# Performance work log

Hardware: AMD Instinct MI355X
Metric: run time of the kernel (lower is better)

## Reference

```python
import jax, jax.numpy as jnp
import numpy as np

NEG_SLOPE_GAT = 0.2   # PyG GATConv default negative_slope
NEG_SLOPE = 0.01      # torch.nn.LeakyReLU default
NUM_AISLES = 20       # aisle_nrs drawn from [0,20); matches aisle_nrs.max()+1


def leaky(x, s):
    return jnp.where(x >= 0, x, s * x)


def gat_conv(x, src, dst, W, a_src, a_dst, b, n_nodes):
    """Single-head PyG GATConv (self-loops already appended to src/dst)."""
    h = x @ W                                        # [N, C]
    es = h @ a_src                                   # [N]
    ed = h @ a_dst                                   # [N]
    e = leaky(es[src] + ed[dst], NEG_SLOPE_GAT)      # [E] per-edge score
    m = jax.ops.segment_max(e, dst, num_segments=n_nodes)
    w = jnp.exp(e - m[dst])
    z = jax.ops.segment_sum(w, dst, num_segments=n_nodes)
    alpha = w / z[dst]                               # segment softmax over incoming edges
    out = jax.ops.segment_sum(h[src] * alpha[:, None], dst, num_segments=n_nodes)
    return out + b


def setup_inputs() -> dict:
    key = jax.random.key(0)
    ks = jax.random.split(key, 32)
    B, N, E = 16, 2048, 32768
    Fin, H, O, HA = 32, 128, 64, 256

    def glorot(k, shape):
        fan = shape[0] + shape[-1]
        return jax.random.uniform(k, shape, jnp.float32, -1.0, 1.0) * np.sqrt(6.0 / fan)

    inp = {
        "graph_nodes": jax.random.normal(ks[0], (B, N, Fin), jnp.float32),
        "aisle_nrs": jax.random.randint(ks[1], (B, N), 0, NUM_AISLES),
        "graph_edge_links": jax.random.randint(ks[2], (B, 2, E), 0, N),
        "mask": jax.random.randint(ks[3], (B, N), 0, 2),
        "picks_left": jax.random.randint(ks[4], (B,), 0, 100),
        # GAT layer 1: Fin -> H
        "W1": glorot(ks[5], (Fin, H)), "as1": glorot(ks[6], (H,)), "ad1": glorot(ks[7], (H,)), "b1": jnp.zeros((H,), jnp.float32),
        # GAT layer 2: H -> H
        "W2": glorot(ks[8], (H, H)), "as2": glorot(ks[9], (H,)), "ad2": glorot(ks[10], (H,)), "b2": jnp.zeros((H,), jnp.float32),
        # GAT layer 3: H -> O
        "W3": glorot(ks[11], (H, O)), "as3": glorot(ks[12], (O,)), "ad3": glorot(ks[13], (O,)), "b3": jnp.zeros((O,), jnp.float32),
        # post-embedding MLP head
        "lw1": glorot(ks[14], (2 * O, HA)), "lb1": jnp.zeros((HA,), jnp.float32),
        "lw2": glorot(ks[15], (HA, O)), "lb2": jnp.zeros((O,), jnp.float32),
        "lw3": glorot(ks[16], (O, 1)), "lb3": jnp.zeros((1,), jnp.float32),
    }
    return inp


def reference(graph_nodes, aisle_nrs, graph_edge_links, mask, picks_left,
              W1, as1, ad1, b1, W2, as2, ad2, b2, W3, as3, ad3, b3,
              lw1, lb1, lw2, lb2, lw3, lb3):
    B, N, Fin = graph_nodes.shape
    NT = B * N
    x = graph_nodes.reshape(NT, Fin)

    # batch the graphs: offset per-graph edge indices, append self-loops
    off = (jnp.arange(B) * N)[:, None]
    src = (graph_edge_links[:, 0, :] + off).reshape(-1)
    dst = (graph_edge_links[:, 1, :] + off).reshape(-1)
    loops = jnp.arange(NT)
    src = jnp.concatenate([src, loops])
    dst = jnp.concatenate([dst, loops])

    x = gat_conv(x, src, dst, W1, as1, ad1, b1, NT)
    x = gat_conv(x, src, dst, W2, as2, ad2, b2, NT)
    x = gat_conv(x, src, dst, W3, as3, ad3, b3, NT)

    # scatter-mean aisle embedding
    batch_idx = jnp.repeat(jnp.arange(B), N)
    aid = aisle_nrs.reshape(-1) + batch_idx * NUM_AISLES   # [NT]
    S = B * NUM_AISLES
    ssum = jax.ops.segment_sum(x, aid, num_segments=S)
    cnt = jax.ops.segment_sum(jnp.ones((NT,), x.dtype), aid, num_segments=S)
    emb = ssum / jnp.maximum(cnt, 1.0)[:, None]

    x = jnp.concatenate([x, emb[aid]], axis=1)             # [NT, 2*O]
    x = leaky(x @ lw1 + lb1, NEG_SLOPE)
    x = leaky(x @ lw2 + lb2, NEG_SLOPE)
    x = (x @ lw3 + lb3).reshape(B, N)

    logits = jnp.where(mask != 0, x, -jnp.inf)
    return jax.nn.softmax(logits, axis=1)
```

## Files before the change

kernel.cpp:

```cpp
#include <hip/hip_runtime.h>
#include <hip/hip_bf16.h>
#include <math.h>

#define BATCH 16
#define NNODE 2048
#define EPG   32768
#define NT    (BATCH * NNODE)
#define ET    (BATCH * EPG + NT)
#define NUM_AISLES 20
#define SEG   (BATCH * NUM_AISLES)
#define NEG_GAT 0.2f
#define NEG_MLP 0.01f
#define ACHUNK 8
#define CAP 64

typedef __attribute__((ext_vector_type(8))) short s16x8;
typedef __attribute__((ext_vector_type(4))) float f32x4;

__device__ __forceinline__ void split_bf16(float v, unsigned short& hi, unsigned short& lo) {
    unsigned int u = __float_as_uint(v);
    unsigned int r = u + 0x7FFFu + ((u >> 16) & 1u);
    hi = (unsigned short)(r >> 16);
    float fh = __uint_as_float(((unsigned int)hi) << 16);
    float rem = v - fh;
    unsigned int u2 = __float_as_uint(rem);
    unsigned int r2 = u2 + 0x7FFFu + ((u2 >> 16) & 1u);
    lo = (unsigned short)(r2 >> 16);
}

__device__ __forceinline__ void decode_edge(int e, const int* __restrict__ links,
                                            int& s, int& d) {
    if (e < BATCH * EPG) {
        int b = e >> 15;
        int i = e & (EPG - 1);
        const int* pb = links + (size_t)b * 2 * EPG;
        s = pb[i] + (b << 11);
        d = pb[EPG + i] + (b << 11);
    } else {
        s = d = e - BATCH * EPG;
    }
}

__global__ __launch_bounds__(256) void edge_scatter(const int* __restrict__ links,
                                                    int* __restrict__ cnt,
                                                    int* __restrict__ col_bkt) {
    int e = blockIdx.x * 256 + threadIdx.x;
    if (e >= ET) return;
    int s, d;
    decode_edge(e, links, s, d);
    int pos = atomicAdd(&cnt[d], 1);
    if (pos < CAP) col_bkt[d * CAP + pos] = s;
}

template <int K, int NOUT, int COLS, bool LEAKY, bool ATTN, bool FINAL, bool CONCAT>
__global__ __launch_bounds__(256) void gemm_mfma(const float* __restrict__ A,
                                                 const float* __restrict__ W,
                                                 const float* __restrict__ bias,
                                                 float* __restrict__ out,
                                                 const float* __restrict__ a_src,
                                                 const float* __restrict__ a_dst,
                                                 float* __restrict__ es,
                                                 float* __restrict__ ed,
                                                 const float* __restrict__ emb,
                                                 const int* __restrict__ aisle,
                                                 const float* __restrict__ lw3,
                                                 const float* __restrict__ lb3,
                                                 const int* __restrict__ mask,
                                                 float* __restrict__ logits) {
    constexpr int BM = 64;
    constexpr int C = COLS / 16;
    constexpr int LDA = 40;

    __shared__ unsigned short Ah[BM * LDA], Al[BM * LDA];
    __shared__ unsigned short Wh[COLS * LDA], Wl[COLS * LDA];

    const int tid = threadIdx.x;
    const int wave = tid >> 6, lane = tid & 63;
    const int quad = lane >> 4, l15 = lane & 15;
    const int row0 = blockIdx.x * BM;
    const int c0 = blockIdx.y * COLS;

    f32x4 acc[C];
#pragma unroll
    for (int c = 0; c < C; ++c)
#pragma unroll
        for (int v = 0; v < 4; ++v) acc[c][v] = 0.f;

    const int arow = tid >> 2;
    const int aq = tid & 3;

    for (int kc = 0; kc < K; kc += 32) {
        {
            const int node = row0 + arow;
            const int off = kc + aq * 8;
            const float* srcp;
            if constexpr (CONCAT) {
                if (off < 64) {
                    srcp = A + (size_t)node * 64 + off;
                } else {
                    int g = node >> 11;
                    srcp = emb + ((size_t)(g * NUM_AISLES + aisle[node])) * 64 + (off - 64);
                }
            } else {
                srcp = A + (size_t)node * K + off;
            }
            unsigned short* dh = Ah + arow * LDA + aq * 8;
            unsigned short* dl = Al + arow * LDA + aq * 8;
#pragma unroll
            for (int q = 0; q < 2; ++q) {
                float4 v = ((const float4*)srcp)[q];
                unsigned short h0, l0, h1, l1, h2, l2, h3, l3;
                split_bf16(v.x, h0, l0);
                split_bf16(v.y, h1, l1);
                split_bf16(v.z, h2, l2);
                split_bf16(v.w, h3, l3);
                dh[q * 4 + 0] = h0; dh[q * 4 + 1] = h1; dh[q * 4 + 2] = h2; dh[q * 4 + 3] = h3;
                dl[q * 4 + 0] = l0; dl[q * 4 + 1] = l1; dl[q * 4 + 2] = l2; dl[q * 4 + 3] = l3;
            }
        }
        for (int i = tid; i < 32 * COLS; i += 256) {
            int k = i / COLS;
            int n = i - k * COLS;
            unsigned short h, l;
            split_bf16(W[(size_t)(kc + k) * NOUT + c0 + n], h, l);
            Wh[n * LDA + k] = h;
            Wl[n * LDA + k] = l;
        }
        __syncthreads();
        {
            int m = wave * 16 + l15;
            s16x8 ah = *(const s16x8*)&Ah[m * LDA + quad * 8];
            s16x8 al = *(const s16x8*)&Al[m * LDA + quad * 8];
#pragma unroll
            for (int c = 0; c < C; ++c) {
                int n = c * 16 + l15;
                s16x8 wh = *(const s16x8*)&Wh[n * LDA + quad * 8];
                s16x8 wl = *(const s16x8*)&Wl[n * LDA + quad * 8];
                acc[c] = __builtin_amdgcn_mfma_f32_16x16x32_bf16(ah, wh, acc[c], 0, 0, 0);
                acc[c] = __builtin_amdgcn_mfma_f32_16x16x32_bf16(ah, wl, acc[c], 0, 0, 0);
                acc[c] = __builtin_amdgcn_mfma_f32_16x16x32_bf16(al, wh, acc[c], 0, 0, 0);
            }
        }
        __syncthreads();
    }
    if constexpr (FINAL) {
#pragma unroll
        for (int reg = 0; reg < 4; ++reg) {
            float p = 0.f;
#pragma unroll
            for (int c = 0; c < C; ++c) {
                int colx = c * 16 + l15;
                float v = acc[c][reg] + bias[colx];
                v = v >= 0.f ? v : NEG_MLP * v;
                p += v * lw3[colx];
            }
#pragma unroll
            for (int mk = 1; mk < 16; mk <<= 1) p += __shfl_xor(p, mk, 64);
            if (l15 == 0) {
                int row = row0 + wave * 16 + quad * 4 + reg;
                float lg = p + lb3[0];
                logits[row] = (mask[row] != 0) ? lg : -INFINITY;
            }
        }
    } else {
#pragma unroll
        for (int c = 0; c < C; ++c) {
            int colx = c0 + c * 16 + l15;
            float bv = bias ? bias[colx] : 0.f;
#pragma unroll
            for (int reg = 0; reg < 4; ++reg) {
                int row = row0 + wave * 16 + quad * 4 + reg;
                float v = acc[c][reg] + bv;
                if (LEAKY) v = v >= 0.f ? v : NEG_MLP * v;
                out[(size_t)row * NOUT + colx] = v;
            }
        }
        if constexpr (ATTN) {
#pragma unroll
            for (int reg = 0; reg < 4; ++reg) {
                float ps = 0.f, pd = 0.f;
#pragma unroll
                for (int c = 0; c < C; ++c) {
                    int colx = c * 16 + l15;
                    float v = acc[c][reg];
                    ps += v * a_src[colx];
                    pd += v * a_dst[colx];
                }
#pragma unroll
                for (int mk = 1; mk < 16; mk <<= 1) {
                    ps += __shfl_xor(ps, mk, 64);
                    pd += __shfl_xor(pd, mk, 64);
                }
                if (l15 == 0) {
                    int row = row0 + wave * 16 + quad * 4 + reg;
                    es[row] = ps;
                    ed[row] = pd;
                }
            }
        }
    }
}

template <int HD>
__global__ __launch_bounds__(256) void gat_aggregate(const float* __restrict__ h,
                                                     const float* __restrict__ es,
                                                     const float* __restrict__ ed,
                                                     const int* __restrict__ cnt,
                                                     const int* __restrict__ col_bkt,
                                                     const float* __restrict__ bias,
                                                     float* __restrict__ out) {
    int node = (blockIdx.x * 256 + threadIdx.x) >> 6;
    int lane = threadIdx.x & 63;
    if (node >= NT) return;
    int deg = cnt[node];
    deg = deg < CAP ? deg : CAP;
    float edv = ed[node];

    float e0 = -INFINITY;
    int c0v = 0;
    if (lane < deg) {
        c0v = col_bkt[node * CAP + lane];
        float e = es[c0v] + edv;
        e0 = e >= 0.f ? e : NEG_GAT * e;
    }
    float m = e0;
#pragma unroll
    for (int off = 32; off; off >>= 1) m = fmaxf(m, __shfl_xor(m, off, 64));
    float z = __expf(e0 - m);
#pragma unroll
    for (int off = 32; off; off >>= 1) z += __shfl_xor(z, off, 64);
    float w0 = __expf(e0 - m) / z;

    int half = lane >> 5;
    int l31 = lane & 31;
    if (HD == 128) {
        float ax = 0.f, ay = 0.f, az = 0.f, aw = 0.f;
        for (int jj = 0; jj < deg; jj += 2) {
            int j2 = jj + half;
            int s = __shfl(c0v, j2, 64);
            float w = __shfl(w0, j2, 64);
            float4 v = *(const float4*)(h + (size_t)s * 128 + l31 * 4);
            ax += w * v.x; ay += w * v.y; az += w * v.z; aw += w * v.w;
        }
        ax += __shfl_xor(ax, 32, 64);
        ay += __shfl_xor(ay, 32, 64);
        az += __shfl_xor(az, 32, 64);
        aw += __shfl_xor(aw, 32, 64);
        if (half == 0) {
            float4 bv = *(const float4*)(bias + l31 * 4);
            float4 o;
            o.x = ax + bv.x; o.y = ay + bv.y; o.z = az + bv.z; o.w = aw + bv.w;
            *(float4*)(out + (size_t)node * 128 + l31 * 4) = o;
        }
    } else {
        float ax = 0.f, ay = 0.f;
        for (int jj = 0; jj < deg; jj += 2) {
            int j2 = jj + half;
            int s = __shfl(c0v, j2, 64);
            float w = __shfl(w0, j2, 64);
            float2 v = *(const float2*)(h + (size_t)s * 64 + l31 * 2);
            ax += w * v.x; ay += w * v.y;
        }
        ax += __shfl_xor(ax, 32, 64);
        ay += __shfl_xor(ay, 32, 64);
        if (half == 0) {
            float2 bv = *(const float2*)(bias + l31 * 2);
            float2 o;
            o.x = ax + bv.x; o.y = ay + bv.y;
            *(float2*)(out + (size_t)node * 64 + l31 * 2) = o;
        }
    }
}

__global__ __launch_bounds__(256) void aisle_partial(const float* __restrict__ x3,
                                                     const int* __restrict__ aisle,
                                                     float* __restrict__ psum,
                                                     int* __restrict__ pcnt) {
    int g = blockIdx.x >> 3;
    int ch = blockIdx.x & 7;
    int f = threadIdx.x & 63;
    int stripe = threadIdx.x >> 6;

    __shared__ float sacc[4][NUM_AISLES][64];
    __shared__ int scnt[4][NUM_AISLES];
    for (int i = threadIdx.x; i < 4 * NUM_AISLES * 64; i += 256)
        ((float*)sacc)[i] = 0.f;
    for (int i = threadIdx.x; i < 4 * NUM_AISLES; i += 256)
        ((int*)scnt)[i] = 0;
    __syncthreads();

    const int* ai = aisle + g * NNODE;
    const float* xg = x3 + (size_t)g * NNODE * 64;
    int n0 = ch * 256 + stripe * 64;
#pragma unroll 4
    for (int i = 0; i < 64; ++i) {
        int n = n0 + i;
        int a = ai[n];
        float v = xg[(size_t)n * 64 + f];
        sacc[stripe][a][f] += v;
        if (f == 0) scnt[stripe][a]++;
    }
    __syncthreads();

    for (int i = threadIdx.x; i < NUM_AISLES * 64; i += 256) {
        int a = i >> 6, ff = i & 63;
        psum[((size_t)blockIdx.x * NUM_AISLES + a) * 64 + ff] =
            sacc[0][a][ff] + sacc[1][a][ff] + sacc[2][a][ff] + sacc[3][a][ff];
    }
    for (int i = threadIdx.x; i < NUM_AISLES; i += 256) {
        pcnt[blockIdx.x * NUM_AISLES + i] =
            scnt[0][i] + scnt[1][i] + scnt[2][i] + scnt[3][i];
    }
}

__global__ __launch_bounds__(256) void aisle_reduce(const float* __restrict__ psum,
                                                    const int* __restrict__ pcnt,
                                                    float* __restrict__ emb) {
    int idx = blockIdx.x * 256 + threadIdx.x;
    if (idx >= SEG * 64) return;
    int seg = idx >> 6;
    int f = idx & 63;
    int g = seg / NUM_AISLES;
    int a = seg - g * NUM_AISLES;
    float s = 0.f;
    int c = 0;
#pragma unroll
    for (int ch = 0; ch < ACHUNK; ++ch) {
        int blk = g * ACHUNK + ch;
        s += psum[((size_t)blk * NUM_AISLES + a) * 64 + f];
        c += pcnt[blk * NUM_AISLES + a];
    }
    emb[idx] = s / fmaxf((float)c, 1.0f);
}

__global__ __launch_bounds__(256) void softmax_kernel(const float* __restrict__ logits,
                                                      float* __restrict__ out) {
    int b = blockIdx.x;
    const float* lr = logits + b * NNODE;
    __shared__ float red[4], redz[4];
    float m = -INFINITY;
    for (int i = threadIdx.x; i < NNODE; i += 256) m = fmaxf(m, lr[i]);
#pragma unroll
    for (int off = 32; off; off >>= 1) m = fmaxf(m, __shfl_xor(m, off, 64));
    if ((threadIdx.x & 63) == 0) red[threadIdx.x >> 6] = m;
    __syncthreads();
    m = fmaxf(fmaxf(red[0], red[1]), fmaxf(red[2], red[3]));
    float z = 0.f;
    for (int i = threadIdx.x; i < NNODE; i += 256) z += __expf(lr[i] - m);
#pragma unroll
    for (int off = 32; off; off >>= 1) z += __shfl_xor(z, off, 64);
    if ((threadIdx.x & 63) == 0) redz[threadIdx.x >> 6] = z;
    __syncthreads();
    z = redz[0] + redz[1] + redz[2] + redz[3];
    float invz = 1.0f / z;
    for (int i = threadIdx.x; i < NNODE; i += 256) {
        float v = lr[i];
        out[b * NNODE + i] = (v == -INFINITY) ? 0.f : __expf(v - m) * invz;
    }
}


extern "C" void kernel_launch(void* const* d_in, const int* in_sizes, int n_in,
                              void* d_out, int out_size, void* d_ws, size_t ws_size,
                              hipStream_t stream) {
    const float* gn   = (const float*)d_in[0];
    const int* aisle  = (const int*)d_in[1];
    const int* links  = (const int*)d_in[2];
    const int* mask   = (const int*)d_in[3];
    const float* W1  = (const float*)d_in[5];
    const float* as1 = (const float*)d_in[6];
    const float* ad1 = (const float*)d_in[7];
    const float* b1  = (const float*)d_in[8];
    const float* W2  = (const float*)d_in[9];
    const float* as2 = (const float*)d_in[10];
    const float* ad2 = (const float*)d_in[11];
    const float* b2  = (const float*)d_in[12];
    const float* W3  = (const float*)d_in[13];
    const float* as3 = (const float*)d_in[14];
    const float* ad3 = (const float*)d_in[15];
    const float* b3  = (const float*)d_in[16];
    const float* lw1 = (const float*)d_in[17];
    const float* lb1 = (const float*)d_in[18];
    const float* lw2 = (const float*)d_in[19];
    const float* lb2 = (const float*)d_in[20];
    const float* lw3 = (const float*)d_in[21];
    const float* lb3 = (const float*)d_in[22];
    float* out = (float*)d_out;

    float* ws = (float*)d_ws;
    float* h      = ws;
    float* xb     = h + (size_t)NT * 128;
    float* es     = xb + (size_t)NT * 128;
    float* ed     = es + NT;
    float* emb    = ed + NT;
    float* y1     = emb + SEG * 64;
    float* y2     = y1 + (size_t)NT * 256;
    float* logits = y2 + (size_t)NT * 64;
    float* psum   = logits + NT;
    int* pcnt     = (int*)(psum + 128 * NUM_AISLES * 64);
    int* row_ptr  = pcnt + 128 * NUM_AISLES;
    int* cnt      = row_ptr + NT + 1;
    int* col_bkt  = (int*)y2;

    const int EB = (ET + 255) / 256;

    hipMemsetAsync(cnt, 0, NT * sizeof(int), stream);
    edge_scatter<<<EB, 256, 0, stream>>>(links, cnt, col_bkt);

    gemm_mfma<32, 128, 128, false, true, false, false><<<dim3(NT / 64, 1), 256, 0, stream>>>(
        gn, W1, nullptr, h, as1, ad1, es, ed, nullptr, nullptr, nullptr, nullptr, nullptr, nullptr);
    gat_aggregate<128><<<NT / 4, 256, 0, stream>>>(h, es, ed, cnt, col_bkt, b1, xb);

    gemm_mfma<128, 128, 128, false, true, false, false><<<dim3(NT / 64, 1), 256, 0, stream>>>(
        xb, W2, nullptr, h, as2, ad2, es, ed, nullptr, nullptr, nullptr, nullptr, nullptr, nullptr);
    gat_aggregate<128><<<NT / 4, 256, 0, stream>>>(h, es, ed, cnt, col_bkt, b2, xb);

    gemm_mfma<128, 64, 64, false, true, false, false><<<dim3(NT / 64, 1), 256, 0, stream>>>(
        xb, W3, nullptr, h, as3, ad3, es, ed, nullptr, nullptr, nullptr, nullptr, nullptr, nullptr);
    gat_aggregate<64><<<NT / 4, 256, 0, stream>>>(h, es, ed, cnt, col_bkt, b3, xb);

    aisle_partial<<<BATCH * ACHUNK, 256, 0, stream>>>(xb, aisle, psum, pcnt);
    aisle_reduce<<<(SEG * 64 + 255) / 256, 256, 0, stream>>>(psum, pcnt, emb);

    gemm_mfma<128, 256, 128, true, false, false, true><<<dim3(NT / 64, 2), 256, 0, stream>>>(
        xb, lw1, lb1, y1, nullptr, nullptr, nullptr, nullptr, emb, aisle, nullptr, nullptr, nullptr, nullptr);
    gemm_mfma<256, 64, 64, true, false, true, false><<<dim3(NT / 64, 1), 256, 0, stream>>>(
        y1, lw2, lb2, y2, nullptr, nullptr, nullptr, nullptr, nullptr, nullptr, lw3, lb3, mask, logits);

    softmax_kernel<<<BATCH, 256, 0, stream>>>(logits, out);
}
```

Baseline: 338.0 us.

## Map graphs to XCDs in scatter/aggregate and widen per-lane gather to 4 edges

Block indices in edge_scatter and gat_aggregate are remapped so that all blocks touching one graph land on the same XCD (blockIdx & 7), which keeps that graph's h rows, counters and buckets in one XCD's L2. The aggregation loop now processes four neighbours per iteration, with each 16-lane group loading 8 (or 4) contiguous floats. This halves the loop trip count and adds more loads in flight, at the cost of an extra shuffle-reduction stage. The remap hardcodes the grid size and assumes round-robin block dispatch across XCDs.

```diff
diff --git a/kernel.cpp b/kernel.cpp
--- a/kernel.cpp
+++ b/kernel.cpp
@@ -28,26 +28,26 @@
     lo = (unsigned short)(r2 >> 16);
 }
 
-__device__ __forceinline__ void decode_edge(int e, const int* __restrict__ links,
-                                            int& s, int& d) {
-    if (e < BATCH * EPG) {
-        int b = e >> 15;
-        int i = e & (EPG - 1);
-        const int* pb = links + (size_t)b * 2 * EPG;
-        s = pb[i] + (b << 11);
-        d = pb[EPG + i] + (b << 11);
-    } else {
-        s = d = e - BATCH * EPG;
-    }
-}
-
 __global__ __launch_bounds__(256) void edge_scatter(const int* __restrict__ links,
                                                     int* __restrict__ cnt,
                                                     int* __restrict__ col_bkt) {
-    int e = blockIdx.x * 256 + threadIdx.x;
-    if (e >= ET) return;
+    int b = blockIdx.x;
     int s, d;
-    decode_edge(e, links, s, d);
+    if (b < 2048) {
+        int xcd = b & 7, idx = b >> 3;
+        int g = xcd * 2 + (idx >> 7);
+        int chunk = idx & 127;
+        int i = chunk * 256 + threadIdx.x;
+        const int* pb = links + (size_t)g * 2 * EPG;
+        s = pb[i] + (g << 11);
+        d = pb[EPG + i] + (g << 11);
+    } else {
+        int b2 = b - 2048;
+        int xcd = b2 & 7, idx = b2 >> 3;
+        int g = xcd * 2 + (idx >> 3);
+        int chunk = idx & 7;
+        s = d = g * NNODE + chunk * 256 + threadIdx.x;
+    }
     int pos = atomicAdd(&cnt[d], 1);
     if (pos < CAP) col_bkt[d * CAP + pos] = s;
 }
@@ -209,9 +209,11 @@
                                                      const int* __restrict__ col_bkt,
                                                      const float* __restrict__ bias,
                                                      float* __restrict__ out) {
-    int node = (blockIdx.x * 256 + threadIdx.x) >> 6;
+    int b = blockIdx.x;
+    int xcd = b & 7, q = b >> 3;
+    int graph = xcd * 2 + (q >> 9);
+    int node = graph * NNODE + (q & 511) * 4 + (threadIdx.x >> 6);
     int lane = threadIdx.x & 63;
-    if (node >= NT) return;
     int deg = cnt[node];
     deg = deg < CAP ? deg : CAP;
     float edv = ed[node];
@@ -231,43 +233,55 @@
     for (int off = 32; off; off >>= 1) z += __shfl_xor(z, off, 64);
     float w0 = __expf(e0 - m) / z;
 
-    int half = lane >> 5;
-    int l31 = lane & 31;
+    const int quad = lane >> 4, l15 = lane & 15;
     if (HD == 128) {
-        float ax = 0.f, ay = 0.f, az = 0.f, aw = 0.f;
-        for (int jj = 0; jj < deg; jj += 2) {
-            int j2 = jj + half;
+        float a0 = 0.f, a1 = 0.f, a2 = 0.f, a3 = 0.f;
+        float a4 = 0.f, a5 = 0.f, a6 = 0.f, a7 = 0.f;
+        for (int jj = 0; jj < deg; jj += 4) {
+            int j2 = jj + quad;
             int s = __shfl(c0v, j2, 64);
             float w = __shfl(w0, j2, 64);
-            float4 v = *(const float4*)(h + (size_t)s * 128 + l31 * 4);
-            ax += w * v.x; ay += w * v.y; az += w * v.z; aw += w * v.w;
-        }
-        ax += __shfl_xor(ax, 32, 64);
-        ay += __shfl_xor(ay, 32, 64);
-        az += __shfl_xor(az, 32, 64);
-        aw += __shfl_xor(aw, 32, 64);
-        if (half == 0) {
-            float4 bv = *(const float4*)(bias + l31 * 4);
-            float4 o;
-            o.x = ax + bv.x; o.y = ay + bv.y; o.z = az + bv.z; o.w = aw + bv.w;
-            *(float4*)(out + (size_t)node * 128 + l31 * 4) = o;
+            const float* base = h + (size_t)s * 128 + l15 * 8;
+            float4 v0 = *(const float4*)base;
+            float4 v1 = *(const float4*)(base + 4);
+            a0 += w * v0.x; a1 += w * v0.y; a2 += w * v0.z; a3 += w * v0.w;
+            a4 += w * v1.x; a5 += w * v1.y; a6 += w * v1.z; a7 += w * v1.w;
+        }
+#pragma unroll
+        for (int off = 16; off <= 32; off <<= 1) {
+            a0 += __shfl_xor(a0, off, 64); a1 += __shfl_xor(a1, off, 64);
+            a2 += __shfl_xor(a2, off, 64); a3 += __shfl_xor(a3, off, 64);
+            a4 += __shfl_xor(a4, off, 64); a5 += __shfl_xor(a5, off, 64);
+            a6 += __shfl_xor(a6, off, 64); a7 += __shfl_xor(a7, off, 64);
+        }
+        if (quad == 0) {
+            const float* bb = bias + l15 * 8;
+            float4 o0, o1;
+            o0.x = a0 + bb[0]; o0.y = a1 + bb[1]; o0.z = a2 + bb[2]; o0.w = a3 + bb[3];
+            o1.x = a4 + bb[4]; o1.y = a5 + bb[5]; o1.z = a6 + bb[6]; o1.w = a7 + bb[7];
+            float* op = out + (size_t)node * 128 + l15 * 8;
+            *(float4*)op = o0;
+            *(float4*)(op + 4) = o1;
         }
     } else {
-        float ax = 0.f, ay = 0.f;
-        for (int jj = 0; jj < deg; jj += 2) {
-            int j2 = jj + half;
+        float a0 = 0.f, a1 = 0.f, a2 = 0.f, a3 = 0.f;
+        for (int jj = 0; jj < deg; jj += 4) {
+            int j2 = jj + quad;
             int s = __shfl(c0v, j2, 64);
             float w = __shfl(w0, j2, 64);
-            float2 v = *(const float2*)(h + (size_t)s * 64 + l31 * 2);
-            ax += w * v.x; ay += w * v.y;
-        }
-        ax += __shfl_xor(ax, 32, 64);
-        ay += __shfl_xor(ay, 32, 64);
-        if (half == 0) {
-            float2 bv = *(const float2*)(bias + l31 * 2);
-            float2 o;
-            o.x = ax + bv.x; o.y = ay + bv.y;
-            *(float2*)(out + (size_t)node * 64 + l31 * 2) = o;
+            float4 v = *(const float4*)(h + (size_t)s * 64 + l15 * 4);
+            a0 += w * v.x; a1 += w * v.y; a2 += w * v.z; a3 += w * v.w;
+        }
+#pragma unroll
+        for (int off = 16; off <= 32; off <<= 1) {
+            a0 += __shfl_xor(a0, off, 64); a1 += __shfl_xor(a1, off, 64);
+            a2 += __shfl_xor(a2, off, 64); a3 += __shfl_xor(a3, off, 64);
+        }
+        if (quad == 0) {
+            const float* bb = bias + l15 * 4;
+            float4 o;
+            o.x = a0 + bb[0]; o.y = a1 + bb[1]; o.z = a2 + bb[2]; o.w = a3 + bb[3];
+            *(float4*)(out + (size_t)node * 64 + l15 * 4) = o;
         }
     }
 }
```

Result: faster. 325.2 us (-3.8%).
